# Performance work log

Hardware: AMD Instinct MI355X
Metric: run time of the kernel (lower is better)

The kernel has to match this reference:

```python
import jax, jax.numpy as jnp
import numpy as np

KERNEL = 5
STRIDE = 1
D = 32
B = 8
L = 2048


def setup_inputs() -> dict:
    key = jax.random.key(0)
    k1, k2, k3, k4, k5 = jax.random.split(key, 5)
    dd = D * D
    scale_dense = 1.0 / np.sqrt(dd)
    scale_attn = 1.0 / np.sqrt(dd * KERNEL)
    return {
        "inputs": jax.random.normal(k1, (B, L, D, D), dtype=jnp.float32),
        "W_dense": jax.random.normal(k2, (dd, dd), dtype=jnp.float32) * scale_dense,
        "b_dense": jax.random.normal(k3, (dd,), dtype=jnp.float32) * scale_dense,
        "W_attn": jax.random.normal(k4, (KERNEL, dd * KERNEL), dtype=jnp.float32) * scale_attn,
        "b_attn": jax.random.normal(k5, (KERNEL,), dtype=jnp.float32) * scale_attn,
    }


def _forward(inputs, W_dense, b_dense, W_attn, b_attn):
    b, l, d, _ = inputs.shape
    pad = KERNEL - 1
    pad_left, pad_right = pad // 2, (pad - 1) // 2 + 1

    # Linear2D: linear over flattened d*d dims
    h = jnp.einsum('blde,fe->bldf',
                   inputs.reshape(b, l, d * d)[..., None, :].squeeze(-2).reshape(b, l, 1, d * d),
                   W_dense).reshape(b, l, d * d) + b_dense
    h = h.reshape(b, l, d, d)

    # pad_identity: pad seq dim with identity matrices (neutral for matrix chain)
    eye = jnp.broadcast_to(jnp.eye(d, dtype=inputs.dtype), (b, 1, d, d))
    h_pad = jnp.concatenate(
        [jnp.broadcast_to(eye, (b, pad_left, d, d)), h,
         jnp.broadcast_to(eye, (b, pad_right, d, d))], axis=1)

    out_len = (l + pad - KERNEL) // STRIDE + 1
    # unfold(dim=1, size=KERNEL, step=STRIDE) -> [b, out_len, d, d, KERNEL]
    h_unf = jnp.stack([h_pad[:, k * 1: k + out_len * STRIDE: STRIDE][:, :out_len]
                       for k in range(KERNEL)], axis=-1)

    attention_inputs = h_unf.reshape(b, out_len, d * d * KERNEL)
    scores = attention_inputs @ W_attn.T + b_attn          # [b, out_len, KERNEL]
    alpha = jax.nn.softmax(jax.nn.leaky_relu(scores, 0.01), axis=2)
    alpha = alpha.reshape(b, out_len, 1, 1, KERNEL)

    h_attn = alpha * h_unf                                  # [b, out_len, d, d, KERNEL]
    out = h_attn[..., 0]
    for i in range(1, KERNEL):
        out = jnp.einsum('bcij,bcjk->bcik', out, h_attn[..., i])
    return out


def reference(inputs, W_dense, b_dense, W_attn, b_attn):
    return _forward(inputs, W_dense, b_dense, W_attn, b_attn)
```

## Files before the change

kernel.cpp:

```cpp
#include <hip/hip_runtime.h>
#include <stdint.h>

typedef float  f32x4  __attribute__((ext_vector_type(4)));
typedef float  f32x16 __attribute__((ext_vector_type(16)));
typedef short  s16x8  __attribute__((ext_vector_type(8)));
typedef unsigned short u16x4 __attribute__((ext_vector_type(4)));

#define LPAD 2052

__device__ __forceinline__ float bf2f(unsigned short u){
  unsigned v = ((unsigned)u) << 16;
  return __builtin_bit_cast(float, v);
}
__device__ __forceinline__ unsigned short f2bf(float f){
  unsigned u = __builtin_bit_cast(unsigned, f);
  u += 0x7fffu + ((u >> 16) & 1u);
  return (unsigned short)(u >> 16);
}
__device__ __forceinline__ unsigned cvt_pk_bf16(float lo, float hi){
  unsigned r;
  asm volatile("v_cvt_pk_bf16_f32 %0, %1, %2" : "=v"(r) : "v"(lo), "v"(hi));
  return r;
}

__global__ void k_cvt(const float* __restrict__ src, unsigned short* __restrict__ dst, int n4){
  int i = blockIdx.x * 256 + threadIdx.x;
  if (i >= n4) return;
  f32x4 v = ((const f32x4*)src)[i];
  u16x4 o;
  o[0] = f2bf(v[0]); o[1] = f2bf(v[1]); o[2] = f2bf(v[2]); o[3] = f2bf(v[3]);
  ((u16x4*)dst)[i] = o;
}

__global__ void k_eye(unsigned short* __restrict__ H){
  int t = blockIdx.x * 256 + threadIdx.x;
  int b = t >> 12;
  int r = t & 4095;
  int which = r >> 10;
  int ij = r & 1023;
  int p = (which < 2) ? which : (2048 + which);
  H[((size_t)(b * LPAD + p) << 10) + ij] = ((ij >> 5) == (ij & 31)) ? 0x3F80 : 0;
}

__global__ void k_wprep(const float* __restrict__ Wa, unsigned short* __restrict__ Wa2g){
  int t = blockIdx.x * 256 + threadIdx.x;
  int col = t >> 10, k = t & 1023;
  int f = col / 5, kk = col - 5 * f;
  unsigned short v = 0;
  if (col < 25) v = f2bf(Wa[f * 5120 + k * 5 + kk]);
  Wa2g[t] = v;
}

#define MFMA16 __builtin_amdgcn_mfma_f32_16x16x32_bf16

__global__ __launch_bounds__(512, 2) void k_gemm8(const unsigned short* __restrict__ A,
                                                  const unsigned short* __restrict__ Bw,
                                                  const float* __restrict__ bias,
                                                  unsigned short* __restrict__ H){
  __shared__ __align__(128) unsigned short lds[65536];
  const int tid = threadIdx.x;
  const int wid = tid >> 6, l = tid & 63;
  const int wm2 = wid >> 2, wn2 = wid & 3;
  const int lm = l & 15, lk = l >> 4;
  const int hb = blockIdx.x;
  const int xcd = hb & 7, sl = hb >> 3;
  const int bm = xcd * 8 + (sl >> 2), bn = sl & 3;
  const int M0 = bm * 256, N0 = bn * 256;

  const unsigned ko0 = (unsigned)((lk ^ (lm & 7)) << 4);
  const unsigned ko1 = ko0 ^ 64u;
  const unsigned aB0 = (unsigned)wm2 * 16384;
  const unsigned bB0 = 32768u + (unsigned)(wn2 >> 1) * 16384;
  const unsigned rB  = (((unsigned)(wn2 & 1)) * 64 + lm) * 128;
  const unsigned rA  = (unsigned)lm * 128;

  f32x4 acc[8][4] = {};
  s16x8 af[4][2], bf0[2][2], bf1[2][2];

  #define STAGE_HALF(panelRow, mat, bufbase)                                         \
    { _Pragma("unroll")                                                              \
      for (int j = 0; j < 2; j++){                                                   \
        unsigned d = (unsigned)(j * 512 + tid) * 16;                                 \
        unsigned row = d >> 7;                                                       \
        unsigned srcC = ((d >> 4) & 7u) ^ (row & 7u);                                \
        const unsigned short* g = (mat) + (size_t)((panelRow) + row) * 1024          \
                                  + ktK + srcC * 8;                                  \
        __builtin_amdgcn_global_load_lds(                                            \
          (const __attribute__((address_space(1))) void*)g,                          \
          (__attribute__((address_space(3))) void*)&lds[((bufbase) + d) >> 1],       \
          16, 0, 0);                                                                 \
      } }
  #define STAGE_Q(b, kt, q)                                                          \
    { const int ktK = (kt) * 64;                                                     \
      if ((q) == 0)      STAGE_HALF(M0,       A,  (b)*65536u)                        \
      else if ((q) == 1) STAGE_HALF(M0+128,   A,  (b)*65536u+16384u)                 \
      else if ((q) == 2) STAGE_HALF(N0,       Bw, (b)*65536u+32768u)                 \
      else               STAGE_HALF(N0+128,   Bw, (b)*65536u+49152u) }

  #define RD_A(mh) { _Pragma("unroll")                                               \
    for (int m = 0; m < 4; m++){                                                     \
      af[m][0] = *(const s16x8*)&lds[(aB + rA + ((mh)*4+m)*2048u + ko0) >> 1];       \
      af[m][1] = *(const s16x8*)&lds[(aB + rA + ((mh)*4+m)*2048u + ko1) >> 1]; } }
  #define RD_B(dst, nh) { _Pragma("unroll")                                          \
    for (int n = 0; n < 2; n++){                                                     \
      dst[n][0] = *(const s16x8*)&lds[(bB + rB + ((nh)*2+n)*2048u + ko0) >> 1];      \
      dst[n][1] = *(const s16x8*)&lds[(bB + rB + ((nh)*2+n)*2048u + ko1) >> 1]; } }
  #define MM(mo, no, bfr) { _Pragma("unroll")                                        \
    for (int m = 0; m < 4; m++){ _Pragma("unroll")                                   \
      for (int n = 0; n < 2; n++){                                                   \
        acc[(mo)+m][(no)+n] = MFMA16(af[m][0], bfr[n][0], acc[(mo)+m][(no)+n], 0,0,0); \
        acc[(mo)+m][(no)+n] = MFMA16(af[m][1], bfr[n][1], acc[(mo)+m][(no)+n], 0,0,0); } } }
  #define BARA    { __builtin_amdgcn_s_barrier(); asm volatile("s_waitcnt lgkmcnt(0)":::"memory"); __builtin_amdgcn_sched_barrier(0); }
  #define BARA_NL { __builtin_amdgcn_s_barrier(); __builtin_amdgcn_sched_barrier(0); }
  #define BARB    { __builtin_amdgcn_s_barrier(); __builtin_amdgcn_sched_barrier(0); }

  STAGE_Q(0, 0, 0); STAGE_Q(0, 0, 1); STAGE_Q(0, 0, 2); STAGE_Q(0, 0, 3);
  __builtin_amdgcn_sched_barrier(0);
  STAGE_Q(1, 1, 0);
  __builtin_amdgcn_sched_barrier(0);
  asm volatile("s_waitcnt vmcnt(2)" ::: "memory");
  __builtin_amdgcn_s_barrier();
  __builtin_amdgcn_sched_barrier(0);

  #pragma unroll 1
  for (int i = 0; i < 8; i++){
    const int ktA = 2 * i + 1;
    const int ktB = 2 * i + 2;
    const int ktC = 2 * i + 3;
    unsigned aB = aB0, bB = bB0;
    RD_A(0); RD_B(bf0, 0);
    STAGE_Q(1, ktA, 1);
    BARA; __builtin_amdgcn_s_setprio(1); MM(0, 0, bf0); __builtin_amdgcn_s_setprio(0); BARB;
    RD_B(bf1, 1);
    STAGE_Q(1, ktA, 2);
    BARA; __builtin_amdgcn_s_setprio(1); MM(0, 2, bf1); __builtin_amdgcn_s_setprio(0); BARB;
    RD_A(1);
    STAGE_Q(1, ktA, 3);
    BARA; __builtin_amdgcn_s_setprio(1); MM(4, 2, bf1); __builtin_amdgcn_s_setprio(0); BARB;
    if (ktB < 16) STAGE_Q(0, ktB, 0);
    BARA_NL; __builtin_amdgcn_s_setprio(1); MM(4, 0, bf0); __builtin_amdgcn_s_setprio(0);
    if (i == 7) { asm volatile("s_waitcnt vmcnt(0)" ::: "memory"); }
    else        { asm volatile("s_waitcnt vmcnt(2)" ::: "memory"); }
    BARB;
    aB = 65536u + aB0; bB = 65536u + bB0;
    RD_A(0); RD_B(bf0, 0);
    if (ktB < 16) STAGE_Q(0, ktB, 1);
    BARA; __builtin_amdgcn_s_setprio(1); MM(0, 0, bf0); __builtin_amdgcn_s_setprio(0); BARB;
    RD_B(bf1, 1);
    if (ktB < 16) STAGE_Q(0, ktB, 2);
    BARA; __builtin_amdgcn_s_setprio(1); MM(0, 2, bf1); __builtin_amdgcn_s_setprio(0); BARB;
    RD_A(1);
    if (ktB < 16) STAGE_Q(0, ktB, 3);
    BARA; __builtin_amdgcn_s_setprio(1); MM(4, 2, bf1); __builtin_amdgcn_s_setprio(0); BARB;
    if (ktC < 16) STAGE_Q(1, ktC, 0);
    BARA_NL; __builtin_amdgcn_s_setprio(1); MM(4, 0, bf0); __builtin_amdgcn_s_setprio(0);
    if (i < 7) { asm volatile("s_waitcnt vmcnt(2)" ::: "memory"); }
    BARB;
  }

  float bv[4];
  #pragma unroll
  for (int n = 0; n < 4; n++) bv[n] = bias[N0 + wn2 * 64 + n * 16 + lm];
  #pragma unroll
  for (int m = 0; m < 8; m++){
    #pragma unroll
    for (int r = 0; r < 4; r++){
      int gm = M0 + wm2 * 128 + m * 16 + lk * 4 + r;
      int bb = gm >> 11, li = gm & 2047;
      unsigned short* orow = H + ((size_t)(bb * LPAD + 2 + li) << 10);
      #pragma unroll
      for (int n = 0; n < 4; n++){
        orow[N0 + wn2 * 64 + n * 16 + lm] = f2bf(acc[m][n][r] + bv[n]);
      }
    }
  }
  #undef STAGE_HALF
  #undef STAGE_Q
  #undef RD_A
  #undef RD_B
  #undef MM
  #undef BARA
  #undef BARA_NL
  #undef BARB
}

__global__ __launch_bounds__(256) void k_part(const unsigned short* __restrict__ H,
                                              const unsigned short* __restrict__ Wa2g,
                                              float* __restrict__ part){
  __shared__ unsigned short sB[32768];
  const int tid = threadIdx.x;
  const int wv = tid >> 6, l = tid & 63;
  const int lm = l & 15, lk = l >> 4;
  #pragma unroll
  for (int j = 0; j < 16; j++){
    unsigned d = (unsigned)(j * 256 + tid) * 16;
    unsigned col = d >> 11;
    unsigned srcC = ((d >> 4) & 127u) ^ (col & 7u);
    const unsigned short* g = Wa2g + col * 1024 + srcC * 8;
    __builtin_amdgcn_global_load_lds((const __attribute__((address_space(1))) void*)g,
                                     (__attribute__((address_space(3))) void*)&sB[d >> 1],
                                     16, 0, 0);
  }
  __syncthreads();
  const int rbase = blockIdx.x * 128 + wv * 32;
  f32x4 acc[2][2] = {};
  for (int kk = 0; kk < 1024; kk += 32){
    s16x8 aF[2], bF[2];
    #pragma unroll
    for (int m = 0; m < 2; m++)
      aF[m] = *(const s16x8*)(H + (size_t)(rbase + m * 16 + lm) * 1024 + kk + lk * 8);
    #pragma unroll
    for (int n = 0; n < 2; n++){
      unsigned col = (unsigned)(n * 16 + lm);
      unsigned c = (unsigned)(kk >> 3) + (unsigned)lk;
      bF[n] = *(const s16x8*)&sB[(col * 2048u + ((c ^ (col & 7u)) << 4)) >> 1];
    }
    #pragma unroll
    for (int m = 0; m < 2; m++){
      #pragma unroll
      for (int n = 0; n < 2; n++)
        acc[m][n] = MFMA16(aF[m], bF[n], acc[m][n], 0, 0, 0);
    }
  }
  #pragma unroll
  for (int m = 0; m < 2; m++){
    #pragma unroll
    for (int r = 0; r < 4; r++){
      int row = rbase + m * 16 + lk * 4 + r;
      #pragma unroll
      for (int n = 0; n < 2; n++)
        part[(size_t)row * 32 + n * 16 + lm] = acc[m][n][r];
    }
  }
}

__global__ void k_alpha(const float* __restrict__ part, const float* __restrict__ battn,
                        float* __restrict__ sprod){
  int t = blockIdx.x * 256 + threadIdx.x;
  if (t >= 16384) return;
  int bb = t >> 11, li = t & 2047;
  int pbase = bb * LPAD + li;
  float sc[5];
  #pragma unroll
  for (int f = 0; f < 5; f++){
    float a = battn[f];
    #pragma unroll
    for (int k = 0; k < 5; k++)
      a += part[(size_t)(pbase + k) * 32 + f * 5 + k];
    sc[f] = (a > 0.f) ? a : 0.01f * a;
  }
  float m = sc[0];
  #pragma unroll
  for (int f = 1; f < 5; f++) m = fmaxf(m, sc[f]);
  float e0 = expf(sc[0] - m), e1 = expf(sc[1] - m), e2 = expf(sc[2] - m),
        e3 = expf(sc[3] - m), e4 = expf(sc[4] - m);
  float ssum = e0 + e1 + e2 + e3 + e4;
  float inv = 1.f / ssum;
  float inv2 = inv * inv;
  sprod[t] = (e0 * e1 * e2 * e3 * e4) * inv2 * inv2 * inv;
}

__global__ __launch_bounds__(256) void k_chain(const unsigned short* __restrict__ H,
                                               const float* __restrict__ sp,
                                               float* __restrict__ out){
  const int tid = threadIdx.x;
  const int w = tid >> 6, l = tid & 63;
  const int blk = (blockIdx.x & 7) * 512 + (blockIdx.x >> 3);
  const int pos = blk * 4 + w;
  const int bb = pos >> 11, li = pos & 2047;
  const unsigned short* hbase = H + ((size_t)(bb * LPAD + li) << 10);
  const int col = l & 31;
  const int kh = (l >> 5) << 3;

  const unsigned short* h4 = hbase + 4 * 1024;
  unsigned q0, q1, q2, q3, q4, q5, q6, q7;
  {
    #define LD2(kk) ((unsigned)h4[(kk) * 32 + col] | ((unsigned)h4[((kk) + 1) * 32 + col] << 16))
    q0 = LD2(kh + 0);  q1 = LD2(kh + 2);  q2 = LD2(kh + 4);  q3 = LD2(kh + 6);
    q4 = LD2(kh + 16); q5 = LD2(kh + 18); q6 = LD2(kh + 20); q7 = LD2(kh + 22);
    #undef LD2
  }
  union { unsigned u[4]; s16x8 v; } ub0, ub1;
  ub0.u[0] = q0; ub0.u[1] = q1; ub0.u[2] = q2; ub0.u[3] = q3;
  ub1.u[0] = q4; ub1.u[1] = q5; ub1.u[2] = q6; ub1.u[3] = q7;
  s16x8 Bf0 = ub0.v, Bf1 = ub1.v;

  f32x16 acc;
  #pragma unroll
  for (int st = 0; st < 4; st++){
    const int km = 3 - st;
    const unsigned short* hA = hbase + (km << 10);
    s16x8 A0 = *(const s16x8*)(hA + col * 32 + kh);
    s16x8 A1 = *(const s16x8*)(hA + col * 32 + kh + 16);
    f32x16 z = {0,0,0,0,0,0,0,0,0,0,0,0,0,0,0,0};
    acc = __builtin_amdgcn_mfma_f32_32x32x16_bf16(A0, Bf0, z,   0, 0, 0);
    acc = __builtin_amdgcn_mfma_f32_32x32x16_bf16(A1, Bf1, acc, 0, 0, 0);
    if (st < 3){
      unsigned d0 = cvt_pk_bf16(acc[0],  acc[1]);
      unsigned d1 = cvt_pk_bf16(acc[2],  acc[3]);
      unsigned d2 = cvt_pk_bf16(acc[4],  acc[5]);
      unsigned d3 = cvt_pk_bf16(acc[6],  acc[7]);
      unsigned d4 = cvt_pk_bf16(acc[8],  acc[9]);
      unsigned d5 = cvt_pk_bf16(acc[10], acc[11]);
      unsigned d6 = cvt_pk_bf16(acc[12], acc[13]);
      unsigned d7 = cvt_pk_bf16(acc[14], acc[15]);
      unsigned p0 = __shfl_xor(d0, 32, 64);
      unsigned p1 = __shfl_xor(d1, 32, 64);
      unsigned p2 = __shfl_xor(d2, 32, 64);
      unsigned p3 = __shfl_xor(d3, 32, 64);
      unsigned p4 = __shfl_xor(d4, 32, 64);
      unsigned p5 = __shfl_xor(d5, 32, 64);
      unsigned p6 = __shfl_xor(d6, 32, 64);
      unsigned p7 = __shfl_xor(d7, 32, 64);
      const bool lo = (l < 32);
      ub0.u[0] = lo ? d0 : p2;  ub0.u[1] = lo ? d1 : p3;
      ub0.u[2] = lo ? p0 : d2;  ub0.u[3] = lo ? p1 : d3;
      ub1.u[0] = lo ? d4 : p6;  ub1.u[1] = lo ? d5 : p7;
      ub1.u[2] = lo ? p4 : d6;  ub1.u[3] = lo ? p5 : d7;
      Bf0 = ub0.v; Bf1 = ub1.v;
    }
  }

  const float sv = sp[pos];
  float* ob = out + ((size_t)pos << 10);
  #pragma unroll
  for (int t = 0; t < 16; t++){
    int row = (t & 3) + 8 * (t >> 2) + ((l >> 5) << 2);
    ob[row * 32 + col] = sv * acc[t];
  }
}

extern "C" void kernel_launch(void* const* d_in, const int* in_sizes, int n_in,
                              void* d_out, int out_size, void* d_ws, size_t ws_size,
                              hipStream_t stream){
  const float* X  = (const float*)d_in[0];
  const float* Wd = (const float*)d_in[1];
  const float* bd = (const float*)d_in[2];
  const float* Wa = (const float*)d_in[3];
  const float* ba = (const float*)d_in[4];
  float* out = (float*)d_out;

  char* ws = (char*)d_ws;
  unsigned short* Hpad = (unsigned short*)ws;
  unsigned short* Wbf  = (unsigned short*)(ws + 33619968);
  float*          sprod= (float*)(ws + 33619968 + 2097152);
  unsigned short* Wa2g = (unsigned short*)(ws + 33619968 + 2097152 + 65536);
  unsigned short* Xbf  = (unsigned short*)d_out;
  float*          part = (float*)((char*)d_out + 33554432);

  k_cvt<<<16384, 256, 0, stream>>>(X, Xbf, 4194304);
  k_cvt<<<1024, 256, 0, stream>>>(Wd, Wbf, 262144);
  k_eye<<<128, 256, 0, stream>>>(Hpad);
  k_wprep<<<128, 256, 0, stream>>>(Wa, Wa2g);
  k_gemm8<<<256, 512, 0, stream>>>(Xbf, Wbf, bd, Hpad);
  k_part<<<129, 256, 0, stream>>>(Hpad, Wa2g, part);
  k_alpha<<<64, 256, 0, stream>>>(part, ba, sprod);
  k_chain<<<4096, 256, 0, stream>>>(Hpad, sprod, out);
}
```

Measured before the change: 97.48 us.

## Fuse fp32-to-bf16 input conversion into GEMM A-tile staging

Drops the standalone conversion kernel for the 64 MB fp32 input. The GEMM now loads fp32 A tiles into registers, packs them to bf16 and writes them swizzled into LDS, while B still uses direct global-to-LDS loads. This removes one full write and re-read pass of the activation matrix. In exchange the A path goes through registers (more VGPR pressure at 2 blocks/CU), the prefetch depth is reduced, and each half-iteration now waits on vmcnt(0), which may expose memory latency.

```diff
diff --git a/kernel.cpp b/kernel.cpp
--- a/kernel.cpp
+++ b/kernel.cpp
@@ -5,6 +5,7 @@
 typedef float  f32x16 __attribute__((ext_vector_type(16)));
 typedef short  s16x8  __attribute__((ext_vector_type(8)));
 typedef unsigned short u16x4 __attribute__((ext_vector_type(4)));
+typedef unsigned int   u32x2 __attribute__((ext_vector_type(2)));
 
 #define LPAD 2052
 
@@ -53,7 +54,7 @@
 
 #define MFMA16 __builtin_amdgcn_mfma_f32_16x16x32_bf16
 
-__global__ __launch_bounds__(512, 2) void k_gemm8(const unsigned short* __restrict__ A,
+__global__ __launch_bounds__(512, 2) void k_gemm8(const float* __restrict__ X,
                                                   const unsigned short* __restrict__ Bw,
                                                   const float* __restrict__ bias,
                                                   unsigned short* __restrict__ H){
@@ -76,85 +77,99 @@
 
   f32x4 acc[8][4] = {};
   s16x8 af[4][2], bf0[2][2], bf1[2][2];
-
-  #define STAGE_HALF(panelRow, mat, bufbase)                                         \
-    { _Pragma("unroll")                                                              \
-      for (int j = 0; j < 2; j++){                                                   \
-        unsigned d = (unsigned)(j * 512 + tid) * 16;                                 \
-        unsigned row = d >> 7;                                                       \
-        unsigned srcC = ((d >> 4) & 7u) ^ (row & 7u);                                \
-        const unsigned short* g = (mat) + (size_t)((panelRow) + row) * 1024          \
-                                  + ktK + srcC * 8;                                  \
-        __builtin_amdgcn_global_load_lds(                                            \
-          (const __attribute__((address_space(1))) void*)g,                          \
-          (__attribute__((address_space(3))) void*)&lds[((bufbase) + d) >> 1],       \
-          16, 0, 0);                                                                 \
-      } }
-  #define STAGE_Q(b, kt, q)                                                          \
-    { const int ktK = (kt) * 64;                                                     \
-      if ((q) == 0)      STAGE_HALF(M0,       A,  (b)*65536u)                        \
-      else if ((q) == 1) STAGE_HALF(M0+128,   A,  (b)*65536u+16384u)                 \
-      else if ((q) == 2) STAGE_HALF(N0,       Bw, (b)*65536u+32768u)                 \
-      else               STAGE_HALF(N0+128,   Bw, (b)*65536u+49152u) }
-
-  #define RD_A(mh) { _Pragma("unroll")                                               \
-    for (int m = 0; m < 4; m++){                                                     \
-      af[m][0] = *(const s16x8*)&lds[(aB + rA + ((mh)*4+m)*2048u + ko0) >> 1];       \
+  f32x4 axr[8];
+
+  #define AL_TILE(kt) { const int ktK = (kt) * 64; _Pragma("unroll")                  \
+    for (int j = 0; j < 8; j++){                                                      \
+      unsigned e = (unsigned)(j * 512 + tid);                                         \
+      axr[j] = *(const f32x4*)(X + (size_t)(M0 + (e >> 4)) * 1024 + ktK + (e & 15u) * 4u); } }
+
+  #define AW_TILE(bufbase) { _Pragma("unroll")                                        \
+    for (int j = 0; j < 8; j++){                                                      \
+      unsigned e = (unsigned)(j * 512 + tid);                                         \
+      unsigned row = e >> 4;                                                          \
+      unsigned half = row >> 7, r7 = row & 127u;                                      \
+      unsigned chunk = (e & 15u) >> 1;                                                \
+      unsigned off = (e & 1u) * 8u;                                                   \
+      unsigned d = (bufbase) + half * 16384u + r7 * 128u                              \
+                   + ((chunk ^ (r7 & 7u)) << 4) + off;                                \
+      u32x2 pk;                                                                       \
+      pk[0] = cvt_pk_bf16(axr[j][0], axr[j][1]);                                      \
+      pk[1] = cvt_pk_bf16(axr[j][2], axr[j][3]);                                      \
+      *(u32x2*)&lds[d >> 1] = pk; } }
+
+  #define BS_HALF(kt, h, bufbase) { const int ktK = (kt) * 64; _Pragma("unroll")      \
+    for (int j = 0; j < 2; j++){                                                      \
+      unsigned d = (unsigned)(j * 512 + tid) * 16;                                    \
+      unsigned row = d >> 7;                                                          \
+      unsigned srcC = ((d >> 4) & 7u) ^ (row & 7u);                                   \
+      const unsigned short* g = Bw + (size_t)(N0 + (h) * 128 + row) * 1024            \
+                                + ktK + srcC * 8;                                     \
+      __builtin_amdgcn_global_load_lds(                                               \
+        (const __attribute__((address_space(1))) void*)g,                             \
+        (__attribute__((address_space(3))) void*)&lds[((bufbase) + 32768u + (h) * 16384u + d) >> 1], \
+        16, 0, 0); } }
+
+  #define RD_A(mh) { _Pragma("unroll")                                                \
+    for (int m = 0; m < 4; m++){                                                      \
+      af[m][0] = *(const s16x8*)&lds[(aB + rA + ((mh)*4+m)*2048u + ko0) >> 1];        \
       af[m][1] = *(const s16x8*)&lds[(aB + rA + ((mh)*4+m)*2048u + ko1) >> 1]; } }
-  #define RD_B(dst, nh) { _Pragma("unroll")                                          \
-    for (int n = 0; n < 2; n++){                                                     \
-      dst[n][0] = *(const s16x8*)&lds[(bB + rB + ((nh)*2+n)*2048u + ko0) >> 1];      \
+  #define RD_B(dst, nh) { _Pragma("unroll")                                           \
+    for (int n = 0; n < 2; n++){                                                      \
+      dst[n][0] = *(const s16x8*)&lds[(bB + rB + ((nh)*2+n)*2048u + ko0) >> 1];       \
       dst[n][1] = *(const s16x8*)&lds[(bB + rB + ((nh)*2+n)*2048u + ko1) >> 1]; } }
-  #define MM(mo, no, bfr) { _Pragma("unroll")                                        \
-    for (int m = 0; m < 4; m++){ _Pragma("unroll")                                   \
-      for (int n = 0; n < 2; n++){                                                   \
-        acc[(mo)+m][(no)+n] = MFMA16(af[m][0], bfr[n][0], acc[(mo)+m][(no)+n], 0,0,0); \
+  #define MM(mo, no, bfr) { _Pragma("unroll")                                         \
+    for (int m = 0; m < 4; m++){ _Pragma("unroll")                                    \
+      for (int n = 0; n < 2; n++){                                                    \
+        acc[(mo)+m][(no)+n] = MFMA16(af[m][0], bfr[n][0], acc[(mo)+m][(no)+n], 0,0,0);  \
         acc[(mo)+m][(no)+n] = MFMA16(af[m][1], bfr[n][1], acc[(mo)+m][(no)+n], 0,0,0); } } }
-  #define BARA    { __builtin_amdgcn_s_barrier(); asm volatile("s_waitcnt lgkmcnt(0)":::"memory"); __builtin_amdgcn_sched_barrier(0); }
-  #define BARA_NL { __builtin_amdgcn_s_barrier(); __builtin_amdgcn_sched_barrier(0); }
-  #define BARB    { __builtin_amdgcn_s_barrier(); __builtin_amdgcn_sched_barrier(0); }
-
-  STAGE_Q(0, 0, 0); STAGE_Q(0, 0, 1); STAGE_Q(0, 0, 2); STAGE_Q(0, 0, 3);
-  __builtin_amdgcn_sched_barrier(0);
-  STAGE_Q(1, 1, 0);
-  __builtin_amdgcn_sched_barrier(0);
-  asm volatile("s_waitcnt vmcnt(2)" ::: "memory");
-  __builtin_amdgcn_s_barrier();
-  __builtin_amdgcn_sched_barrier(0);
+  #define SB0   __builtin_amdgcn_sched_barrier(0);
+  #define BARA    { __builtin_amdgcn_s_barrier(); asm volatile("s_waitcnt lgkmcnt(0)":::"memory"); SB0 }
+  #define BARA_NL { __builtin_amdgcn_s_barrier(); SB0 }
+  #define BARB    { __builtin_amdgcn_s_barrier(); SB0 }
+
+  AL_TILE(0); SB0
+  BS_HALF(0, 0, 0u); BS_HALF(0, 1, 0u); SB0
+  asm volatile("s_waitcnt vmcnt(4)" ::: "memory"); SB0
+  AW_TILE(0u); SB0
+  asm volatile("s_waitcnt vmcnt(0) lgkmcnt(0)" ::: "memory");
+  __builtin_amdgcn_s_barrier(); SB0
 
   #pragma unroll 1
   for (int i = 0; i < 8; i++){
     const int ktA = 2 * i + 1;
     const int ktB = 2 * i + 2;
-    const int ktC = 2 * i + 3;
     unsigned aB = aB0, bB = bB0;
     RD_A(0); RD_B(bf0, 0);
-    STAGE_Q(1, ktA, 1);
+    if (ktA < 16){ AL_TILE(ktA); SB0 BS_HALF(ktA, 0, 65536u); }
     BARA; __builtin_amdgcn_s_setprio(1); MM(0, 0, bf0); __builtin_amdgcn_s_setprio(0); BARB;
     RD_B(bf1, 1);
-    STAGE_Q(1, ktA, 2);
+    if (ktA < 16){ BS_HALF(ktA, 1, 65536u); }
     BARA; __builtin_amdgcn_s_setprio(1); MM(0, 2, bf1); __builtin_amdgcn_s_setprio(0); BARB;
     RD_A(1);
-    STAGE_Q(1, ktA, 3);
+    if (ktA < 16){
+      asm volatile("s_waitcnt vmcnt(4)" ::: "memory"); SB0
+      AW_TILE(65536u);
+    }
     BARA; __builtin_amdgcn_s_setprio(1); MM(4, 2, bf1); __builtin_amdgcn_s_setprio(0); BARB;
-    if (ktB < 16) STAGE_Q(0, ktB, 0);
     BARA_NL; __builtin_amdgcn_s_setprio(1); MM(4, 0, bf0); __builtin_amdgcn_s_setprio(0);
-    if (i == 7) { asm volatile("s_waitcnt vmcnt(0)" ::: "memory"); }
-    else        { asm volatile("s_waitcnt vmcnt(2)" ::: "memory"); }
+    asm volatile("s_waitcnt vmcnt(0)" ::: "memory");
     BARB;
     aB = 65536u + aB0; bB = 65536u + bB0;
     RD_A(0); RD_B(bf0, 0);
-    if (ktB < 16) STAGE_Q(0, ktB, 1);
+    if (ktB < 16){ AL_TILE(ktB); SB0 BS_HALF(ktB, 0, 0u); }
     BARA; __builtin_amdgcn_s_setprio(1); MM(0, 0, bf0); __builtin_amdgcn_s_setprio(0); BARB;
     RD_B(bf1, 1);
-    if (ktB < 16) STAGE_Q(0, ktB, 2);
+    if (ktB < 16){ BS_HALF(ktB, 1, 0u); }
     BARA; __builtin_amdgcn_s_setprio(1); MM(0, 2, bf1); __builtin_amdgcn_s_setprio(0); BARB;
     RD_A(1);
-    if (ktB < 16) STAGE_Q(0, ktB, 3);
+    if (ktB < 16){
+      asm volatile("s_waitcnt vmcnt(4)" ::: "memory"); SB0
+      AW_TILE(0u);
+    }
     BARA; __builtin_amdgcn_s_setprio(1); MM(4, 2, bf1); __builtin_amdgcn_s_setprio(0); BARB;
-    if (ktC < 16) STAGE_Q(1, ktC, 0);
     BARA_NL; __builtin_amdgcn_s_setprio(1); MM(4, 0, bf0); __builtin_amdgcn_s_setprio(0);
-    if (i < 7) { asm volatile("s_waitcnt vmcnt(2)" ::: "memory"); }
+    asm volatile("s_waitcnt vmcnt(0)" ::: "memory");
     BARB;
   }
 
@@ -174,11 +189,13 @@
       }
     }
   }
-  #undef STAGE_HALF
-  #undef STAGE_Q
+  #undef AL_TILE
+  #undef AW_TILE
+  #undef BS_HALF
   #undef RD_A
   #undef RD_B
   #undef MM
+  #undef SB0
   #undef BARA
   #undef BARA_NL
   #undef BARB
@@ -345,14 +362,12 @@
   unsigned short* Wbf  = (unsigned short*)(ws + 33619968);
   float*          sprod= (float*)(ws + 33619968 + 2097152);
   unsigned short* Wa2g = (unsigned short*)(ws + 33619968 + 2097152 + 65536);
-  unsigned short* Xbf  = (unsigned short*)d_out;
   float*          part = (float*)((char*)d_out + 33554432);
 
-  k_cvt<<<16384, 256, 0, stream>>>(X, Xbf, 4194304);
   k_cvt<<<1024, 256, 0, stream>>>(Wd, Wbf, 262144);
   k_eye<<<128, 256, 0, stream>>>(Hpad);
   k_wprep<<<128, 256, 0, stream>>>(Wa, Wa2g);
-  k_gemm8<<<256, 512, 0, stream>>>(Xbf, Wbf, bd, Hpad);
+  k_gemm8<<<256, 512, 0, stream>>>(X, Wbf, bd, Hpad);
   k_part<<<129, 256, 0, stream>>>(Hpad, Wa2g, part);
   k_alpha<<<64, 256, 0, stream>>>(part, ba, sprod);
   k_chain<<<4096, 256, 0, stream>>>(Hpad, sprod, out);
```

Result: slower. 187.6 us (+92.5%).
